# Optimization experiments

Hardware: AMD Instinct MI355X
Metric: run time of the kernel (lower is better)

Reference implementation:

```python
import jax, jax.numpy as jnp
import numpy as np

V_DIM, L_DIM, EMBED, HEADS = 1024, 768, 1024, 16
HEAD_DIM = EMBED // HEADS
SCALE = HEADS ** (-0.5)  # faithful to source: num_heads**-0.5
B, NV, NL = 4, 4096, 256


def _xavier(key, shape):
    fan_in, fan_out = shape[0], shape[1]
    lim = (6.0 / (fan_in + fan_out)) ** 0.5
    return jax.random.uniform(key, shape, jnp.float32, -lim, lim)


def setup_inputs() -> dict:
    key = jax.random.key(0)
    ks = jax.random.split(key, 12)
    inp = {
        'v': jax.random.normal(ks[0], (B, NV, V_DIM), jnp.float32),
        'l': jax.random.normal(ks[1], (B, NL, L_DIM), jnp.float32),
        'attention_mask_l': jnp.ones((B, NL), jnp.int32),
        # weights stored as [in, out] so x @ W
        'W_v2q': _xavier(ks[2], (V_DIM, EMBED)), 'b_v2q': jnp.zeros((EMBED,), jnp.float32),
        'W_l2k': _xavier(ks[3], (L_DIM, EMBED)), 'b_l2k': jnp.zeros((EMBED,), jnp.float32),
        'W_v2v': _xavier(ks[4], (V_DIM, EMBED)), 'b_v2v': jnp.zeros((EMBED,), jnp.float32),
        'W_l2v': _xavier(ks[5], (L_DIM, EMBED)), 'b_l2v': jnp.zeros((EMBED,), jnp.float32),
        'W_v2out': _xavier(ks[6], (EMBED, V_DIM)), 'b_v2out': jnp.zeros((V_DIM,), jnp.float32),
        'W_l2out': _xavier(ks[7], (EMBED, L_DIM)), 'b_l2out': jnp.zeros((L_DIM,), jnp.float32),
    }
    return inp


def _heads(x):
    # [B, N, E] -> [B, H, N, D]
    Bx, N, _ = x.shape
    return x.reshape(Bx, N, HEADS, HEAD_DIM).transpose(0, 2, 1, 3)


def reference(v, l, attention_mask_l, W_v2q, b_v2q, W_l2k, b_l2k, W_v2v, b_v2v,
              W_l2v, b_l2v, W_v2out, b_v2out, W_l2out, b_l2out):
    q = _heads(v @ W_v2q + b_v2q)          # [B,H,Nv,D] vision queries
    k = _heads(l @ W_l2k + b_l2k)          # [B,H,Nl,D] language keys
    val_v = _heads(v @ W_v2v + b_v2v)      # [B,H,Nv,D]
    val_l = _heads(l @ W_l2v + b_l2v)      # [B,H,Nl,D]

    # shared score matrix, reused for both softmax directions
    attn = jnp.einsum('bhqd,bhkd->bhqk', q, k) * SCALE  # [B,H,Nv,Nl]

    # vision attends language: mask invalid language tokens
    mask_bias = jnp.where(attention_mask_l[:, None, None, :] == 0, -1e9, 0.0).astype(attn.dtype)
    attn_v = jax.nn.softmax(attn + mask_bias, axis=-1)   # over Nl
    # language attends vision: softmax over vision axis of the same scores
    attn_l = jax.nn.softmax(attn, axis=-2)               # over Nv

    out_v = jnp.einsum('bhqk,bhkd->bhqd', attn_v, val_l)  # [B,H,Nv,D]
    out_l = jnp.einsum('bhqk,bhqd->bhkd', attn_l, val_v)  # [B,H,Nl,D]

    Bx = v.shape[0]
    out_v = out_v.transpose(0, 2, 1, 3).reshape(Bx, -1, EMBED) @ W_v2out + b_v2out
    out_l = out_l.transpose(0, 2, 1, 3).reshape(Bx, -1, EMBED) @ W_l2out + b_l2out
    return out_v, out_l
```

## Files before the change

### kernel.cpp

```cpp
#include <hip/hip_runtime.h>
#include <hip/hip_bf16.h>

#define EMBED 1024
#define HEADS 16
#define HD 64
#define NVTOK 4096
#define NLTOK 256
#define BATCH 4
#define QSCALE 0.25f

typedef __hip_bfloat16 bf16;
typedef __attribute__((ext_vector_type(8))) short bf16x8;
typedef __attribute__((ext_vector_type(4))) float floatx4;

#define MFMA(a, b, c) __builtin_amdgcn_mfma_f32_16x16x32_bf16((a), (b), (c), 0, 0, 0)

static __device__ __forceinline__ short f2bs(float x) {
  bf16 h = __float2bfloat16(x);
  return *reinterpret_cast<short*>(&h);
}
static __device__ __forceinline__ float b2f(bf16 x) { return __bfloat162float(x); }

typedef const __attribute__((address_space(1))) char ga_char;
typedef __attribute__((address_space(3))) char ls_char;
static __device__ __forceinline__ void load_lds16(const void* g, void* lds) {
  __builtin_amdgcn_global_load_lds((ga_char*)g, (ls_char*)(unsigned)(size_t)(lds), 16, 0, 0);
}

__global__ void detect_dtype(const unsigned* __restrict__ v, int* __restrict__ flag) {
  __shared__ int cnt;
  if (threadIdx.x == 0) cnt = 0;
  __syncthreads();
  unsigned u = v[threadIdx.x];
  int mid = (int)((u >> 7) & 0xFF);
  if (mid >= 110 && mid <= 140) atomicAdd(&cnt, 1);
  __syncthreads();
  if (threadIdx.x == 0) {
    flag[0] = (cnt < 192) ? 1 : 0;
    flag[1] = 0;
  }
}

__global__ void convert_to_bf16_v4(const void* __restrict__ src, bf16* __restrict__ dst,
                                   int n4, const int* __restrict__ flag) {
  int i = blockIdx.x * 256 + threadIdx.x;
  if (i >= n4) return;
  short4 o;
  if (flag[0]) {
    float4 f = ((const float4*)src)[i];
    o.x = f2bs(f.x); o.y = f2bs(f.y); o.z = f2bs(f.z); o.w = f2bs(f.w);
  } else {
    o = ((const short4*)src)[i];
  }
  ((short4*)dst)[i] = o;
}

struct WTArgs {
  const void* src[6];
  bf16* dst[6];
  int R[6];
  int C[6];
  float scale[6];
};
__global__ __launch_bounds__(256) void convert_transpose_all(WTArgs a, const int* __restrict__ flag) {
  __shared__ float tile[32][33];
  const int z = blockIdx.y;
  const int R = a.R[z], C = a.C[z];
  const float sc = a.scale[z];
  const int tpc = C >> 5;
  const int nt = (R >> 5) * tpc;
  const int t = blockIdx.x;
  if (t >= nt) return;
  const int r0 = (t / tpc) << 5, c0 = (t % tpc) << 5;
  {
    const int row = threadIdx.x >> 3, cg = (threadIdx.x & 7) << 2;
    if (flag[0]) {
      float4 f = *(const float4*)((const float*)a.src[z] + (size_t)(r0 + row) * C + c0 + cg);
      tile[row][cg] = f.x * sc; tile[row][cg + 1] = f.y * sc;
      tile[row][cg + 2] = f.z * sc; tile[row][cg + 3] = f.w * sc;
    } else {
      short4 f = *(const short4*)((const short*)a.src[z] + (size_t)(r0 + row) * C + c0 + cg);
      tile[row][cg]     = b2f(*(const bf16*)&f.x) * sc;
      tile[row][cg + 1] = b2f(*(const bf16*)&f.y) * sc;
      tile[row][cg + 2] = b2f(*(const bf16*)&f.z) * sc;
      tile[row][cg + 3] = b2f(*(const bf16*)&f.w) * sc;
    }
  }
  __syncthreads();
  {
    const int col = threadIdx.x >> 3, rg = (threadIdx.x & 7) << 2;
    short4 o;
    o.x = f2bs(tile[rg + 0][col]);
    o.y = f2bs(tile[rg + 1][col]);
    o.z = f2bs(tile[rg + 2][col]);
    o.w = f2bs(tile[rg + 3][col]);
    *(short4*)((short*)a.dst[z] + (size_t)(c0 + col) * R + r0 + rg) = o;
  }
}

struct BArgs {
  const void* src[6];
  bf16* dst[6];
  int n[6];
  float scale[6];
};
__global__ void convert_bias_all(BArgs a, const int* __restrict__ flag) {
  int z = blockIdx.y;
  int i = blockIdx.x * 256 + threadIdx.x;
  if (i >= a.n[z]) return;
  float x = flag[0] ? ((const float*)a.src[z])[i] : b2f(((const bf16*)a.src[z])[i]);
  a.dst[z][i] = __float2bfloat16(x * a.scale[z]);
}

__global__ __launch_bounds__(256) void transpose_vl_heads(const bf16* __restrict__ kv,
                                                          bf16* __restrict__ vlT) {
  __shared__ short t[64][72];
  const int bh = blockIdx.y, b = bh >> 4, h = bh & 15;
  const int nl0 = blockIdx.x << 6;
  const int tid = threadIdx.x;
  {
    const int nl = tid >> 2, dg = (tid & 3) << 4;
    const short* s = (const short*)kv + ((size_t)b * NLTOK + nl0 + nl) * 2048 + 1024 + h * HD + dg;
    *(bf16x8*)&t[nl][dg]     = *(const bf16x8*)s;
    *(bf16x8*)&t[nl][dg + 8] = *(const bf16x8*)(s + 8);
  }
  __syncthreads();
  {
    const int d = tid >> 2, ng = (tid & 3) << 4;
    short* o = (short*)vlT + ((size_t)bh * HD + d) * NLTOK + nl0 + ng;
    short tmp[16];
#pragma unroll
    for (int j = 0; j < 16; j++) tmp[j] = t[ng + j][d];
    *(bf16x8*)o       = *(bf16x8*)&tmp[0];
    *(bf16x8*)(o + 8) = *(bf16x8*)&tmp[8];
  }
}

__global__ __launch_bounds__(256) void gemm_nt(
    const bf16* __restrict__ A, const bf16* __restrict__ Bt,
    const bf16* __restrict__ bias, void* __restrict__ Cout, long long coff,
    int M, int N, int K, float alpha, const int* __restrict__ outf) {
  __shared__ short lds_all[16896];
  short* As = lds_all;
  short* Bs = lds_all + 8192;
  const int f32o = outf[0];
  const int tid = threadIdx.x;
  const int wave = tid >> 6, lane = tid & 63;
  const int bm = blockIdx.x * 128, bn = blockIdx.y * 128;
  const int wr = (wave & 1) * 64, wc = (wave >> 1) * 64;
  const int rl = lane & 15, kg = (lane >> 4) * 8;

  const int srow = wave * 16 + (lane >> 2);
  const int scol = (lane & 3) * 8;
  const short* Ag = (const short*)A + (size_t)(bm + srow) * K + scol;
  const short* Bg = (const short*)Bt + (size_t)(bn + srow) * K + scol;
  short* As0l = &As[wave * 512];
  short* As1l = &As[2048 + wave * 512];
  short* As0h = &As[4096 + wave * 512];
  short* As1h = &As[6144 + wave * 512];
  short* Bs0l = &Bs[wave * 512];
  short* Bs1l = &Bs[2048 + wave * 512];
  short* Bs0h = &Bs[4096 + wave * 512];
  short* Bs1h = &Bs[6144 + wave * 512];
  const size_t rstep = (size_t)64 * K;

  floatx4 acc[4][4];
#pragma unroll
  for (int i = 0; i < 4; i++)
#pragma unroll
    for (int j = 0; j < 4; j++) acc[i][j] = (floatx4){0.f, 0.f, 0.f, 0.f};

  for (int k0 = 0; k0 < K; k0 += 64) {
    __syncthreads();
    load_lds16(Ag + k0, As0l);
    load_lds16(Ag + rstep + k0, As1l);
    load_lds16(Ag + k0 + 32, As0h);
    load_lds16(Ag + rstep + k0 + 32, As1h);
    load_lds16(Bg + k0, Bs0l);
    load_lds16(Bg + rstep + k0, Bs1l);
    load_lds16(Bg + k0 + 32, Bs0h);
    load_lds16(Bg + rstep + k0 + 32, Bs1h);
    __syncthreads();
#pragma unroll
    for (int half = 0; half < 2; half++) {
      const short* Ah = &As[half * 4096];
      const short* Bh = &Bs[half * 4096];
      bf16x8 af[4], bfr[4];
#pragma unroll
      for (int i = 0; i < 4; i++) af[i]  = *(const bf16x8*)&Ah[(wr + i * 16 + rl) * 32 + kg];
#pragma unroll
      for (int j = 0; j < 4; j++) bfr[j] = *(const bf16x8*)&Bh[(wc + j * 16 + rl) * 32 + kg];
#pragma unroll
      for (int i = 0; i < 4; i++)
#pragma unroll
        for (int j = 0; j < 4; j++) acc[i][j] = MFMA(af[i], bfr[j], acc[i][j]);
    }
  }

  const int rg = (lane >> 4) * 4;
  __syncthreads();

  if (!f32o) {
#pragma unroll
    for (int j = 0; j < 4; j++) {
      float bv = b2f(bias[bn + wc + j * 16 + rl]);
#pragma unroll
      for (int i = 0; i < 4; i++)
#pragma unroll
        for (int r = 0; r < 4; r++)
          lds_all[(wr + i * 16 + rg + r) * 132 + wc + j * 16 + rl] =
              f2bs((acc[i][j][r] + bv) * alpha);
    }
    __syncthreads();
#pragma unroll
    for (int it = 0; it < 8; it++) {
      int idx = it * 256 + tid;
      int row = idx >> 4, c = idx & 15;
      bf16x8 o = *(const bf16x8*)&lds_all[row * 132 + c * 8];
      *(bf16x8*)((short*)Cout + coff + (long long)(bm + row) * N + bn + c * 8) = o;
    }
  } else {
    float* Cf = (float*)lds_all;
#pragma unroll
    for (int p = 0; p < 2; p++) {
      if ((wave & 1) == p) {
#pragma unroll
        for (int j = 0; j < 4; j++) {
          float bv = b2f(bias[bn + wc + j * 16 + rl]);
#pragma unroll
          for (int i = 0; i < 4; i++)
#pragma unroll
            for (int r = 0; r < 4; r++)
              Cf[(i * 16 + rg + r) * 132 + wc + j * 16 + rl] = (acc[i][j][r] + bv) * alpha;
        }
      }
      __syncthreads();
#pragma unroll
      for (int it = 0; it < 8; it++) {
        int idx = it * 256 + tid;
        int row = idx >> 5, c = idx & 31;
        float4 o = *(const float4*)&Cf[row * 132 + c * 4];
        *(float4*)((float*)Cout + coff + (long long)(bm + p * 64 + row) * N + bn + c * 4) = o;
      }
      if (p == 0) __syncthreads();
    }
  }
}

#define VMCNT6() do { asm volatile("s_waitcnt vmcnt(6)" ::: "memory"); \
                      __builtin_amdgcn_sched_barrier(0); } while (0)
#define VMCNT0() do { asm volatile("s_waitcnt vmcnt(0)" ::: "memory"); \
                      __builtin_amdgcn_sched_barrier(0); } while (0)

static __device__ __forceinline__ void compute_tile256b(
    const short* __restrict__ Ab, const short* __restrict__ Bb,
    floatx4 (&acc)[4][4], int wm, int wn, int rl, int lg) {
  const int sw = rl & 7;
  bf16x8 a[4][2], b[4][2];
#define LDA(m, kk) (*(const bf16x8*)&Ab[(wm * 64 + (m) * 16 + rl) * 64 + ((((kk) * 4 + lg) ^ sw) * 8)])
#define LDB(n, kk) (*(const bf16x8*)&Bb[(wn * 64 + (n) * 16 + rl) * 64 + ((((kk) * 4 + lg) ^ sw) * 8)])
#pragma unroll
  for (int m = 0; m < 4; m++) { a[m][0] = LDA(m, 0); a[m][1] = LDA(m, 1); }
#pragma unroll
  for (int n = 0; n < 4; n++) { b[n][0] = LDB(n, 0); b[n][1] = LDB(n, 1); }
#pragma unroll
  for (int m = 0; m < 4; m++)
#pragma unroll
    for (int n = 0; n < 4; n++) {
      acc[m][n] = MFMA(a[m][0], b[n][0], acc[m][n]);
      acc[m][n] = MFMA(a[m][1], b[n][1], acc[m][n]);
    }
#undef LDA
#undef LDB
}

__global__ __launch_bounds__(512, 2) void gemm256b_nt(
    const bf16* __restrict__ A, const bf16* __restrict__ Bt,
    const bf16* __restrict__ bias, void* __restrict__ Cout, long long coff,
    int M, int N, int K, float alpha, const int* __restrict__ outf) {
  extern __shared__ short lds[];
  short* A0 = lds;
  short* B0 = lds + 16384;
  short* A1 = lds + 24576;
  short* B1 = lds + 40960;
  const int f32o = outf[0];
  const int tid = threadIdx.x;
  const int wave = tid >> 6, lane = tid & 63;
  const int rl = lane & 15, lg = lane >> 4;
  const int wm = wave >> 1, wn = wave & 1;

  const int nwg = gridDim.x;
  const int nNT = N >> 7;
  int orig = blockIdx.x;
  int qq = nwg >> 3, rr = nwg & 7, xcd = orig & 7, sidx = orig >> 3;
  int swz = (xcd < rr) ? (xcd * (qq + 1) + sidx)
                       : (rr * (qq + 1) + (xcd - rr) * qq + sidx);
  const int bm = (swz / nNT) * 256;
  const int bn = (swz % nNT) * 128;

  const int r8 = lane >> 3;
  const int cgs = (lane & 7) ^ r8;
  const short* ga = (const short*)A + (size_t)(bm + wave * 8 + r8) * K + cgs * 8;
  const short* gb = (const short*)Bt + (size_t)(bn + wave * 8 + r8) * K + cgs * 8;

#define STAGE(LA, LB, k0_) do {                                             \
    _Pragma("unroll")                                                       \
    for (int p = 0; p < 4; p++)                                             \
      load_lds16(ga + (size_t)(p * 64) * K + (k0_), (LA) + wave * 512 + p * 4096); \
    _Pragma("unroll")                                                       \
    for (int p = 0; p < 2; p++)                                             \
      load_lds16(gb + (size_t)(p * 64) * K + (k0_), (LB) + wave * 512 + p * 4096); \
  } while (0)

  floatx4 acc[4][4];
#pragma unroll
  for (int m = 0; m < 4; m++)
#pragma unroll
    for (int n = 0; n < 4; n++) acc[m][n] = (floatx4){0.f, 0.f, 0.f, 0.f};

  const int NT = K >> 6;
  STAGE(A0, B0, 0);
  STAGE(A1, B1, 64);
  int kt = 0;
  for (; kt + 2 < NT; kt += 2) {
    VMCNT6();
    __builtin_amdgcn_s_barrier();
    compute_tile256b(A0, B0, acc, wm, wn, rl, lg);
    __builtin_amdgcn_sched_barrier(0);
    __builtin_amdgcn_s_barrier();
    __builtin_amdgcn_sched_barrier(0);
    STAGE(A0, B0, (kt + 2) * 64);
    VMCNT6();
    __builtin_amdgcn_s_barrier();
    compute_tile256b(A1, B1, acc, wm, wn, rl, lg);
    __builtin_amdgcn_sched_barrier(0);
    __builtin_amdgcn_s_barrier();
    __builtin_amdgcn_sched_barrier(0);
    STAGE(A1, B1, (kt + 3) * 64);
  }
  VMCNT6();
  __builtin_amdgcn_s_barrier();
  compute_tile256b(A0, B0, acc, wm, wn, rl, lg);
  VMCNT0();
  __builtin_amdgcn_s_barrier();
  compute_tile256b(A1, B1, acc, wm, wn, rl, lg);
  __syncthreads();

  if (!f32o) {
#pragma unroll
    for (int n = 0; n < 4; n++) {
      float bv = b2f(bias[bn + wn * 64 + n * 16 + rl]);
#pragma unroll
      for (int m = 0; m < 4; m++)
#pragma unroll
        for (int r2 = 0; r2 < 4; r2++)
          lds[(wm * 64 + m * 16 + lg * 4 + r2) * 136 + wn * 64 + n * 16 + rl] =
              f2bs((acc[m][n][r2] + bv) * alpha);
    }
    __syncthreads();
#pragma unroll
    for (int it = 0; it < 8; it++) {
      int idx2 = it * 512 + tid;
      int row = idx2 >> 4, c = idx2 & 15;
      bf16x8 o = *(const bf16x8*)&lds[row * 136 + c * 8];
      *(bf16x8*)((short*)Cout + coff + (long long)(bm + row) * N + bn + c * 8) = o;
    }
  } else {
    float* Cf = (float*)lds;
#pragma unroll
    for (int pp = 0; pp < 2; pp++) {
      if ((wm >> 1) == pp) {
#pragma unroll
        for (int n = 0; n < 4; n++) {
          float bv = b2f(bias[bn + wn * 64 + n * 16 + rl]);
#pragma unroll
          for (int m = 0; m < 4; m++)
#pragma unroll
            for (int r2 = 0; r2 < 4; r2++)
              Cf[((wm & 1) * 64 + m * 16 + lg * 4 + r2) * 132 + wn * 64 + n * 16 + rl] =
                  (acc[m][n][r2] + bv) * alpha;
        }
      }
      __syncthreads();
#pragma unroll
      for (int it = 0; it < 8; it++) {
        int idx2 = it * 512 + tid;
        int row = idx2 >> 5, c = idx2 & 31;
        float4 o = *(const float4*)&Cf[row * 132 + c * 4];
        *(float4*)((float*)Cout + coff + (long long)(bm + pp * 128 + row) * N + bn + c * 4) = o;
      }
      __syncthreads();
    }
  }
#undef STAGE
}

__global__ __launch_bounds__(256, 3) void attn_fwd_v(
    const bf16* __restrict__ qv,
    const bf16* __restrict__ kv,
    const bf16* __restrict__ vlT,
    const int* __restrict__ mask,
    bf16* __restrict__ ovh,
    float* __restrict__ sfin) {
  __shared__ short kp_lds[256 * 72];
  __shared__ float stf[1024];
  const int tid = threadIdx.x, wave = tid >> 6, lane = tid & 63;
  const int qt = blockIdx.x, bh = blockIdx.y;
  const int b = bh >> 4, h = bh & 15;
  const size_t qrow0 = (size_t)b * NVTOK + qt * 64;
  const size_t krow0 = (size_t)b * NLTOK;
  const int rl = lane & 15, lg = lane >> 4;

#pragma unroll
  for (int it = 0; it < 8; it++) {
    int vv = it * 256 + tid;
    int nl = vv >> 3, c = vv & 7;
    *(bf16x8*)&kp_lds[nl * 72 + c * 8] =
        *(const bf16x8*)((const short*)kv + (krow0 + nl) * 2048 + h * HD + c * 8);
  }
  kp_lds[tid * 72 + 64] = (short)(mask[b * NLTOK + tid] != 0);
  __syncthreads();

  floatx4 sacc[16];
#pragma unroll
  for (int ct = 0; ct < 16; ct++) sacc[ct] = (floatx4){0.f, 0.f, 0.f, 0.f};
  const short* qrow = (const short*)qv + (qrow0 + wave * 16 + rl) * 2048 + h * HD;
  bf16x8 a0 = *(const bf16x8*)(qrow + lg * 8);
  bf16x8 a1 = *(const bf16x8*)(qrow + 32 + lg * 8);
#pragma unroll
  for (int ct = 0; ct < 16; ct++) {
    bf16x8 b0 = *(const bf16x8*)&kp_lds[(ct * 16 + rl) * 72 + lg * 8];
    bf16x8 b1 = *(const bf16x8*)&kp_lds[(ct * 16 + rl) * 72 + 32 + lg * 8];
    sacc[ct] = MFMA(a0, b0, sacc[ct]);
    sacc[ct] = MFMA(a1, b1, sacc[ct]);
  }

  const short* vbase = (const short*)vlT + ((size_t)bh * 64 + wave * 16) * 256;
  bf16x8 vfr[8];
#pragma unroll
  for (int ks = 0; ks < 8; ks++)
    vfr[ks] = *(const bf16x8*)(vbase + (size_t)rl * 256 + ks * 32 + lg * 8);

#pragma unroll
  for (int ct = 0; ct < 16; ct++) {
    float s = __expf(sacc[ct][0]) + __expf(sacc[ct][1]) +
              __expf(sacc[ct][2]) + __expf(sacc[ct][3]);
    s += __shfl_xor(s, 16);
    s += __shfl_xor(s, 32);
    if (lane < 16) stf[wave * 256 + ct * 16 + lane] = s;
  }

  float mb[16];
#pragma unroll
  for (int ct = 0; ct < 16; ct++)
    mb[ct] = kp_lds[(ct * 16 + rl) * 72 + 64] ? 0.0f : -1e9f;

  float rmax[4] = {-1e30f, -1e30f, -1e30f, -1e30f};
#pragma unroll
  for (int ct = 0; ct < 16; ct++)
#pragma unroll
    for (int r = 0; r < 4; r++) {
      sacc[ct][r] += mb[ct];
      rmax[r] = fmaxf(rmax[r], sacc[ct][r]);
    }
#pragma unroll
  for (int r = 0; r < 4; r++) {
    rmax[r] = fmaxf(rmax[r], __shfl_xor(rmax[r], 1));
    rmax[r] = fmaxf(rmax[r], __shfl_xor(rmax[r], 2));
    rmax[r] = fmaxf(rmax[r], __shfl_xor(rmax[r], 4));
    rmax[r] = fmaxf(rmax[r], __shfl_xor(rmax[r], 8));
  }
  float rsum[4] = {0.f, 0.f, 0.f, 0.f};
#pragma unroll
  for (int ct = 0; ct < 16; ct++)
#pragma unroll
    for (int r = 0; r < 4; r++) {
      sacc[ct][r] = __expf(sacc[ct][r] - rmax[r]);
      rsum[r] += sacc[ct][r];
    }
#pragma unroll
  for (int r = 0; r < 4; r++) {
    rsum[r] += __shfl_xor(rsum[r], 1);
    rsum[r] += __shfl_xor(rsum[r], 2);
    rsum[r] += __shfl_xor(rsum[r], 4);
    rsum[r] += __shfl_xor(rsum[r], 8);
    rsum[r] = 1.0f / fmaxf(rsum[r], 1e-20f);
  }
  __syncthreads();

  {
    float s = stf[tid] + stf[256 + tid] + stf[512 + tid] + stf[768 + tid];
    atomicAdd(&sfin[(size_t)bh * 256 + tid], s);
  }

#pragma unroll
  for (int ct = 0; ct < 16; ct++)
#pragma unroll
    for (int r = 0; r < 4; r++)
      kp_lds[(wave * 16 + lg * 4 + r) * 268 + ct * 16 + rl] = f2bs(sacc[ct][r] * rsum[r]);
  __syncthreads();

  floatx4 oacc[4];
#pragma unroll
  for (int mt = 0; mt < 4; mt++) oacc[mt] = (floatx4){0.f, 0.f, 0.f, 0.f};
#pragma unroll
  for (int ks = 0; ks < 8; ks++) {
#pragma unroll
    for (int mt = 0; mt < 4; mt++) {
      bf16x8 af = *(const bf16x8*)&kp_lds[(mt * 16 + rl) * 268 + ks * 32 + lg * 8];
      oacc[mt] = MFMA(af, vfr[ks], oacc[mt]);
    }
  }
  __syncthreads();

#pragma unroll
  for (int mt = 0; mt < 4; mt++)
#pragma unroll
    for (int r = 0; r < 4; r++)
      kp_lds[(mt * 16 + lg * 4 + r) * 72 + wave * 16 + rl] = f2bs(oacc[mt][r]);
  __syncthreads();

#pragma unroll
  for (int pass = 0; pass < 2; pass++) {
    int idx = pass * 256 + tid;
    int row = idx >> 3, c = idx & 7;
    bf16x8 o = *(const bf16x8*)&kp_lds[row * 72 + c * 8];
    *(bf16x8*)((short*)ovh + (qrow0 + row) * EMBED + h * HD + c * 8) = o;
  }
}

__global__ void zero_f32(float* __restrict__ p, int n) {
  int i = blockIdx.x * 256 + threadIdx.x;
  if (i < n) p[i] = 0.f;
}

__global__ __launch_bounds__(256) void attn_fwd_l(
    const bf16* __restrict__ qv,
    const bf16* __restrict__ kv,
    const float* __restrict__ sf,
    float* __restrict__ olacc) {
  __shared__ short k_lds[256 * 72];
  __shared__ short PT[256 * 40];
  __shared__ short vvT[64 * 40];
  __shared__ float sl[256];
  const int tid = threadIdx.x, wave = tid >> 6, lane = tid & 63;
  const int chunk = blockIdx.x, bh = blockIdx.y;
  const int b = bh >> 4, h = bh & 15;
  const size_t krow0 = (size_t)b * NLTOK;
  const size_t qbase = (size_t)b * NVTOK + chunk * 512;
  const int rl = lane & 15, lg = lane >> 4;

#pragma unroll
  for (int it = 0; it < 8; it++) {
    int vvi = it * 256 + tid;
    int nl = vvi >> 3, c = vvi & 7;
    *(bf16x8*)&k_lds[nl * 72 + c * 8] =
        *(const bf16x8*)((const short*)kv + (krow0 + nl) * 2048 + h * HD + c * 8);
  }
  sl[tid] = 1.0f / fmaxf(sf[(size_t)bh * 256 + tid], 1e-20f);
  __syncthreads();

  floatx4 acc[4][4];
#pragma unroll
  for (int rt = 0; rt < 4; rt++)
#pragma unroll
    for (int dt = 0; dt < 4; dt++) acc[rt][dt] = (floatx4){0.f, 0.f, 0.f, 0.f};

  const int qrt = wave & 1, ctb = (wave >> 1) * 8;
  for (int qs = 0; qs < 16; qs++) {
    const short* qrow = (const short*)qv + (qbase + qs * 32 + qrt * 16 + rl) * 2048 + h * HD;
    bf16x8 a0 = *(const bf16x8*)(qrow + lg * 8);
    bf16x8 a1 = *(const bf16x8*)(qrow + 32 + lg * 8);
    floatx4 s8[8];
#pragma unroll
    for (int i = 0; i < 8; i++) {
      int ct = ctb + i;
      bf16x8 b0 = *(const bf16x8*)&k_lds[(ct * 16 + rl) * 72 + lg * 8];
      bf16x8 b1 = *(const bf16x8*)&k_lds[(ct * 16 + rl) * 72 + 32 + lg * 8];
      floatx4 s = (floatx4){0.f, 0.f, 0.f, 0.f};
      s = MFMA(a0, b0, s);
      s = MFMA(a1, b1, s);
      s8[i] = s;
    }
    __syncthreads();
#pragma unroll
    for (int i = 0; i < 8; i++) {
      int col = (ctb + i) * 16 + rl;
      float linv = sl[col];
#pragma unroll
      for (int r = 0; r < 4; r++)
        PT[col * 40 + qrt * 16 + lg * 4 + r] = f2bs(__expf(s8[i][r]) * linv);
    }
    {
      int qq = tid >> 3, c = tid & 7;
      bf16x8 vvv = *(const bf16x8*)((const short*)qv +
                                    (qbase + qs * 32 + qq) * 2048 + 1024 + h * HD + c * 8);
      const short* vp = (const short*)&vvv;
#pragma unroll
      for (int j = 0; j < 8; j++) vvT[(c * 8 + j) * 40 + qq] = vp[j];
    }
    __syncthreads();
#pragma unroll
    for (int rt = 0; rt < 4; rt++) {
      bf16x8 af = *(const bf16x8*)&PT[(wave * 64 + rt * 16 + rl) * 40 + lg * 8];
#pragma unroll
      for (int dt = 0; dt < 4; dt++) {
        bf16x8 bfr = *(const bf16x8*)&vvT[(dt * 16 + rl) * 40 + lg * 8];
        acc[rt][dt] = MFMA(af, bfr, acc[rt][dt]);
      }
    }
  }
#pragma unroll
  for (int rt = 0; rt < 4; rt++)
#pragma unroll
    for (int dt = 0; dt < 4; dt++)
#pragma unroll
      for (int r = 0; r < 4; r++) {
        int nl = wave * 64 + rt * 16 + lg * 4 + r;
        int d = dt * 16 + rl;
        atomicAdd(&olacc[((size_t)b * NLTOK + nl) * EMBED + h * HD + d], acc[rt][dt][r]);
      }
}

__global__ void finalize_out_l(const float* __restrict__ olacc, bf16* __restrict__ olh) {
  int i = blockIdx.x * 256 + threadIdx.x;
  if (i < 1024 * 1024) olh[i] = __float2bfloat16(olacc[i]);
}

extern "C" void kernel_launch(void* const* d_in, const int* in_sizes, int n_in,
                              void* d_out, int out_size, void* d_ws, size_t ws_size,
                              hipStream_t stream) {
  (void)in_sizes; (void)n_in; (void)out_size; (void)ws_size;
  const void* v_raw = d_in[0];
  const void* l_raw = d_in[1];
  const int*  mask  = (const int*)d_in[2];
  const void* W_v2q = d_in[3];  const void* b_v2q = d_in[4];
  const void* W_l2k = d_in[5];  const void* b_l2k = d_in[6];
  const void* W_v2v = d_in[7];  const void* b_v2v = d_in[8];
  const void* W_l2v = d_in[9];  const void* b_l2v = d_in[10];
  const void* W_v2o = d_in[11]; const void* b_v2o = d_in[12];
  const void* W_l2o = d_in[13]; const void* b_l2o = d_in[14];

  static bool lds_attr_ok = false;
  if (!lds_attr_ok) {
    hipFuncSetAttribute((const void*)gemm256b_nt,
                        hipFuncAttributeMaxDynamicSharedMemorySize, 98304);
    lds_attr_ok = true;
  }

  char* ws = (char*)d_ws;
  size_t off = 0;
  auto alloc = [&](size_t bytes) -> void* {
    void* p = ws + off;
    off += (bytes + 255) & ~(size_t)255;
    return p;
  };
  int*  flag   = (int*)alloc(256);
  bf16* vb     = (bf16*)alloc((size_t)16777216 * 2);
  bf16* lb     = (bf16*)alloc((size_t)786432 * 2);
  bf16* b_qv   = (bf16*)alloc(4096);
  bf16* b_kvl  = (bf16*)alloc(4096);
  bf16* bov    = (bf16*)alloc(2048);
  bf16* bol    = (bf16*)alloc(1536);
  bf16* Wqv    = (bf16*)alloc((size_t)2048 * 1024 * 2);
  bf16* Wkvl   = (bf16*)alloc((size_t)2048 * 768 * 2);
  bf16* Wt_v2o = (bf16*)alloc((size_t)1024 * 1024 * 2);
  bf16* Wt_l2o = (bf16*)alloc((size_t)768 * 1024 * 2);
  bf16* qvb    = (bf16*)alloc((size_t)16384 * 2048 * 2);
  bf16* kvb    = (bf16*)alloc((size_t)1024 * 2048 * 2);
  bf16* vlT    = (bf16*)alloc((size_t)64 * 64 * 256 * 2);
  float* sfin  = (float*)alloc((size_t)64 * 256 * 4);
  float* olacc = (float*)alloc((size_t)1024 * 1024 * 4);
  bf16* olh    = (bf16*)alloc((size_t)1024 * 1024 * 2);
  bf16* ovh    = vb;

  detect_dtype<<<1, 256, 0, stream>>>((const unsigned*)v_raw, flag);

  convert_to_bf16_v4<<<16384, 256, 0, stream>>>(v_raw, vb, 4194304, flag);
  convert_to_bf16_v4<<<768, 256, 0, stream>>>(l_raw, lb, 196608, flag);

  BArgs ba;
  ba.src[0] = b_v2q; ba.dst[0] = b_qv;         ba.n[0] = 1024; ba.scale[0] = QSCALE;
  ba.src[1] = b_l2k; ba.dst[1] = b_kvl;        ba.n[1] = 1024; ba.scale[1] = 1.0f;
  ba.src[2] = b_v2v; ba.dst[2] = b_qv + 1024;  ba.n[2] = 1024; ba.scale[2] = 1.0f;
  ba.src[3] = b_l2v; ba.dst[3] = b_kvl + 1024; ba.n[3] = 1024; ba.scale[3] = 1.0f;
  ba.src[4] = b_v2o; ba.dst[4] = bov;          ba.n[4] = 1024; ba.scale[4] = 1.0f;
  ba.src[5] = b_l2o; ba.dst[5] = bol;          ba.n[5] = 768;  ba.scale[5] = 1.0f;
  convert_bias_all<<<dim3(4, 6), 256, 0, stream>>>(ba, flag);

  WTArgs wa;
  wa.src[0] = W_v2q; wa.dst[0] = Wqv;                     wa.R[0] = 1024; wa.C[0] = 1024; wa.scale[0] = QSCALE;
  wa.src[1] = W_l2k; wa.dst[1] = Wkvl;                    wa.R[1] = 768;  wa.C[1] = 1024; wa.scale[1] = 1.0f;
  wa.src[2] = W_v2v; wa.dst[2] = Wqv + (size_t)1024*1024; wa.R[2] = 1024; wa.C[2] = 1024; wa.scale[2] = 1.0f;
  wa.src[3] = W_l2v; wa.dst[3] = Wkvl + (size_t)1024*768; wa.R[3] = 768;  wa.C[3] = 1024; wa.scale[3] = 1.0f;
  wa.src[4] = W_v2o; wa.dst[4] = Wt_v2o;                  wa.R[4] = 1024; wa.C[4] = 1024; wa.scale[4] = 1.0f;
  wa.src[5] = W_l2o; wa.dst[5] = Wt_l2o;                  wa.R[5] = 1024; wa.C[5] = 768;  wa.scale[5] = 1.0f;
  convert_transpose_all<<<dim3(1024, 6), 256, 0, stream>>>(wa, flag);

  zero_f32<<<4161, 256, 0, stream>>>(sfin, 64 * 256 + 1024 * 1024);

  const int* bf16out = flag + 1;
  gemm256b_nt<<<1024, 512, 98304, stream>>>(vb, Wqv, b_qv, qvb, 0, 16384, 2048, 1024, 1.0f, bf16out);
  gemm_nt<<<dim3(8, 16), 256, 0, stream>>>(lb, Wkvl, b_kvl, kvb, 0, 1024, 2048, 768, 1.0f, bf16out);
  transpose_vl_heads<<<dim3(4, 64), 256, 0, stream>>>(kvb, vlT);

  attn_fwd_v<<<dim3(64, 64), 256, 0, stream>>>(qvb, kvb, vlT, mask, ovh, sfin);
  attn_fwd_l<<<dim3(8, 64), 256, 0, stream>>>(qvb, kvb, sfin, olacc);
  finalize_out_l<<<4096, 256, 0, stream>>>(olacc, olh);

  gemm256b_nt<<<512, 512, 98304, stream>>>(ovh, Wt_v2o, bov, d_out, 0, 16384, 1024, 1024, 1.0f, flag);
  gemm_nt<<<dim3(8, 6), 256, 0, stream>>>(olh, Wt_l2o, bol, d_out, 16777216LL, 1024, 768, 1024, 1.0f, flag);
}
```

Measured before the change: 449.9 us.

## Triple-buffer LDS in 256-row GEMM to drop one barrier per k-tile

Changes the big GEMM's shared-memory pipeline from two buffers to a rotating set of three, with one barrier per k-step instead of two. The next global-to-LDS stage is issued before computing the current tile, which should improve overlap and cut synchronisation. LDS use grows from 96 KB to 144 KB per block, which drops occupancy from two blocks per CU to one under the 160 KB LDS limit.

Result: slower. 467.5 us (+3.9%).

```diff
diff --git a/kernel.cpp b/kernel.cpp
--- a/kernel.cpp
+++ b/kernel.cpp
@@ -279,10 +279,6 @@
     const bf16* __restrict__ bias, void* __restrict__ Cout, long long coff,
     int M, int N, int K, float alpha, const int* __restrict__ outf) {
   extern __shared__ short lds[];
-  short* A0 = lds;
-  short* B0 = lds + 16384;
-  short* A1 = lds + 24576;
-  short* B1 = lds + 40960;
   const int f32o = outf[0];
   const int tid = threadIdx.x;
   const int wave = tid >> 6, lane = tid & 63;
@@ -303,13 +299,13 @@
   const short* ga = (const short*)A + (size_t)(bm + wave * 8 + r8) * K + cgs * 8;
   const short* gb = (const short*)Bt + (size_t)(bn + wave * 8 + r8) * K + cgs * 8;
 
-#define STAGE(LA, LB, k0_) do {                                             \
+#define STAGE(BUF, k0_) do {                                                \
     _Pragma("unroll")                                                       \
     for (int p = 0; p < 4; p++)                                             \
-      load_lds16(ga + (size_t)(p * 64) * K + (k0_), (LA) + wave * 512 + p * 4096); \
+      load_lds16(ga + (size_t)(p * 64) * K + (k0_), (BUF) + wave * 512 + p * 4096); \
     _Pragma("unroll")                                                       \
     for (int p = 0; p < 2; p++)                                             \
-      load_lds16(gb + (size_t)(p * 64) * K + (k0_), (LB) + wave * 512 + p * 4096); \
+      load_lds16(gb + (size_t)(p * 64) * K + (k0_), (BUF) + 16384 + wave * 512 + p * 4096); \
   } while (0)
 
   floatx4 acc[4][4];
@@ -318,32 +314,27 @@
 #pragma unroll
     for (int n = 0; n < 4; n++) acc[m][n] = (floatx4){0.f, 0.f, 0.f, 0.f};
 
+  short* cur = lds;
+  short* nxt = lds + 24576;
+  short* fut = lds + 49152;
+
   const int NT = K >> 6;
-  STAGE(A0, B0, 0);
-  STAGE(A1, B1, 64);
-  int kt = 0;
-  for (; kt + 2 < NT; kt += 2) {
+  STAGE(cur, 0);
+  STAGE(nxt, 64);
+  for (int kt = 0; kt < NT - 2; ++kt) {
     VMCNT6();
     __builtin_amdgcn_s_barrier();
-    compute_tile256b(A0, B0, acc, wm, wn, rl, lg);
-    __builtin_amdgcn_sched_barrier(0);
-    __builtin_amdgcn_s_barrier();
-    __builtin_amdgcn_sched_barrier(0);
-    STAGE(A0, B0, (kt + 2) * 64);
-    VMCNT6();
-    __builtin_amdgcn_s_barrier();
-    compute_tile256b(A1, B1, acc, wm, wn, rl, lg);
-    __builtin_amdgcn_sched_barrier(0);
-    __builtin_amdgcn_s_barrier();
-    __builtin_amdgcn_sched_barrier(0);
-    STAGE(A1, B1, (kt + 3) * 64);
+    STAGE(fut, (kt + 2) * 64);
+    compute_tile256b(cur, cur + 16384, acc, wm, wn, rl, lg);
+    short* tmp = cur; cur = nxt; nxt = fut; fut = tmp;
   }
   VMCNT6();
   __builtin_amdgcn_s_barrier();
-  compute_tile256b(A0, B0, acc, wm, wn, rl, lg);
+  compute_tile256b(cur, cur + 16384, acc, wm, wn, rl, lg);
+  { short* tmp = cur; cur = nxt; nxt = fut; fut = tmp; }
   VMCNT0();
   __builtin_amdgcn_s_barrier();
-  compute_tile256b(A1, B1, acc, wm, wn, rl, lg);
+  compute_tile256b(cur, cur + 16384, acc, wm, wn, rl, lg);
   __syncthreads();
 
   if (!f32o) {
@@ -644,7 +635,7 @@
   static bool lds_attr_ok = false;
   if (!lds_attr_ok) {
     hipFuncSetAttribute((const void*)gemm256b_nt,
-                        hipFuncAttributeMaxDynamicSharedMemorySize, 98304);
+                        hipFuncAttributeMaxDynamicSharedMemorySize, 147456);
     lds_attr_ok = true;
   }
 
@@ -700,7 +691,7 @@
   zero_f32<<<4161, 256, 0, stream>>>(sfin, 64 * 256 + 1024 * 1024);
 
   const int* bf16out = flag + 1;
-  gemm256b_nt<<<1024, 512, 98304, stream>>>(vb, Wqv, b_qv, qvb, 0, 16384, 2048, 1024, 1.0f, bf16out);
+  gemm256b_nt<<<1024, 512, 147456, stream>>>(vb, Wqv, b_qv, qvb, 0, 16384, 2048, 1024, 1.0f, bf16out);
   gemm_nt<<<dim3(8, 16), 256, 0, stream>>>(lb, Wkvl, b_kvl, kvb, 0, 1024, 2048, 768, 1.0f, bf16out);
   transpose_vl_heads<<<dim3(4, 64), 256, 0, stream>>>(kvb, vlT);
 
@@ -708,6 +699,6 @@
   attn_fwd_l<<<dim3(8, 64), 256, 0, stream>>>(qvb, kvb, sfin, olacc);
   finalize_out_l<<<4096, 256, 0, stream>>>(olacc, olh);
 
-  gemm256b_nt<<<512, 512, 98304, stream>>>(ovh, Wt_v2o, bov, d_out, 0, 16384, 1024, 1024, 1.0f, flag);
+  gemm256b_nt<<<512, 512, 147456, stream>>>(ovh, Wt_v2o, bov, d_out, 0, 16384, 1024, 1024, 1.0f, flag);
   gemm_nt<<<dim3(8, 6), 256, 0, stream>>>(olh, Wt_l2o, bol, d_out, 16777216LL, 1024, 768, 1024, 1.0f, flag);
 }
```
